# Optimization experiments

Measured on AMD Instinct MI355X. Metric: run time of the kernel, lower is better.

The kernel has to match this reference:

```python
import jax, jax.numpy as jnp
import numpy as np

B, N = 4096, 128
STATE_DIM, GOAL_DIM, OBSTACLE_DIM = 6, 6, 4
VEH = 2 * STATE_DIM + GOAL_DIM  # 18


def setup_inputs() -> dict:
    key = jax.random.key(0)
    ks = jax.random.split(key, 8)
    s = lambda k, shp, fan: jax.random.normal(k, shp, jnp.float32) / np.sqrt(fan)
    return {
        "obs": jax.random.normal(ks[0], (B, 138), jnp.float32),
        "obstacles": jax.random.uniform(ks[1], (B, 5, N), jnp.float32),
        "act": jax.random.normal(ks[2], (B, 2), jnp.float32),
        "ow1": s(ks[3], (22, 256), 22),
        "ob1": jnp.zeros((256,), jnp.float32),
        "ow2": s(ks[4], (256, 256), 256),
        "ob2": jnp.zeros((256,), jnp.float32),
        "qw1": s(ks[5], (396, 256), 396),
        "qb1": jnp.zeros((256,), jnp.float32),
        "qw2": s(ks[6], (256, 256), 256),
        "qb2": jnp.zeros((256,), jnp.float32),
        "qw3": s(ks[7], (256, 1), 256),
        "qb3": jnp.zeros((1,), jnp.float32),
    }


def reference(obs, obstacles, act, ow1, ob1, ow2, ob2, qw1, qb1, qw2, qb2, qw3, qb3):
    # obs: [B, 138]; obstacles: [B, obstacle_dim+1, N]; act: [B, 2]
    veh = obs[:, :VEH]                                 # [B, 18]
    obst_data = obstacles[:, :OBSTACLE_DIM, :]         # [B, 4, N]
    mask = obstacles[:, -1, :]                         # [B, N]
    # per-obstacle features: concat broadcast vehicle state with obstacle data -> [B, N, 22]
    x = jnp.concatenate(
        [jnp.broadcast_to(veh[:, None, :], (veh.shape[0], obst_data.shape[2], VEH)),
         obst_data.transpose(0, 2, 1)], axis=-1)
    # shared obstacle MLP (ReLU on both layers, incl. output_activation)
    h = jax.nn.relu(jnp.einsum("bnf,fh->bnh", x, ow1) + ob1)
    h = jax.nn.relu(jnp.einsum("bnh,hk->bnk", h, ow2) + ob2)  # [B, N, 256]
    # masked sum-pool over obstacle axis
    pooled = jnp.einsum("bnh,bn->bh", h, mask)         # [B, 256]
    comb = jnp.concatenate([obs, pooled, act], axis=-1)  # [B, 396]
    q = jax.nn.relu(comb @ qw1 + qb1)
    q = jax.nn.relu(q @ qw2 + qb2)
    q = q @ qw3 + qb3                                   # [B, 1]
    return jnp.squeeze(q, -1)
```

## Files before the change

kernel.cpp:

```cpp
#include <hip/hip_runtime.h>
#include <hip/hip_bf16.h>


typedef __attribute__((ext_vector_type(8))) short short8;
typedef __attribute__((ext_vector_type(4))) float f32x4;

#define MFMA16(A, B, C) __builtin_amdgcn_mfma_f32_16x16x32_bf16(A, B, C, 0, 0, 0)

__device__ __forceinline__ unsigned short f2b(float f) {
  __hip_bfloat16 h = __float2bfloat16(f);
  return __builtin_bit_cast(unsigned short, h);
}
__device__ __forceinline__ float b2f(unsigned short u) {
  unsigned v = ((unsigned)u) << 16;
  return __builtin_bit_cast(float, v);
}
__device__ __forceinline__ unsigned pk2f(float a, float b) {
  unsigned ua = __builtin_bit_cast(unsigned, a) + 0x8000u;
  unsigned ub = __builtin_bit_cast(unsigned, b) + 0x8000u;
  return __builtin_amdgcn_perm(ub, ua, 0x07060302u);
}

__global__ __launch_bounds__(256) void pack_weights(
    const float* __restrict__ ow1, const float* __restrict__ ow2,
    const float* __restrict__ qw1, const float* __restrict__ qw2,
    unsigned short* __restrict__ ow1q, unsigned short* __restrict__ ow2p,
    unsigned short* __restrict__ qw1h, unsigned short* __restrict__ qw1l,
    unsigned short* __restrict__ qw2h, unsigned short* __restrict__ qw2l) {
  int i = blockIdx.x * 256 + threadIdx.x;
  if (i < 8192) {
    int j = i & 7;
    int l15 = (i >> 3) & 15;
    int quad = (i >> 7) & 3;
    int mt = (i >> 9) & 15;
    int k = quad * 8 + j;
    float v = (k < 22) ? ow1[k * 256 + (mt * 16 + l15)] : 0.f;
    ow1q[i] = f2b(v);
  }
  if (i < 65536) {
    int j = i & 7;
    int n = (i >> 3) & 255;
    int qq = i >> 11;
    int k = (qq >> 2) * 32 + (qq & 3) * 8 + j;
    ow2p[i] = f2b(ow2[k * 256 + n]);
    float w = qw2[k * 256 + n];
    unsigned short h = f2b(w);
    qw2h[i] = h;
    qw2l[i] = f2b(w - b2f(h));
  }
  if (i < 106496) {
    int j = i & 7;
    int n = (i >> 3) & 255;
    int qq = i >> 11;
    int k = (qq >> 2) * 32 + (qq & 3) * 8 + j;
    float w = (k < 396) ? qw1[k * 256 + n] : 0.f;
    unsigned short h = f2b(w);
    qw1h[i] = h;
    qw1l[i] = f2b(w - b2f(h));
  }
}

#define XSTR 40
#define HSTR 272

__global__ __launch_bounds__(512, 4) void obstacle_kernel(
    const float* __restrict__ obs, const float* __restrict__ obstacles,
    const unsigned short* __restrict__ ow1q,
    const unsigned short* __restrict__ ow2p,
    const float* __restrict__ ob1, const float* __restrict__ ob2,
    unsigned short* __restrict__ poolH, unsigned short* __restrict__ poolL) {
  __shared__ __align__(16) unsigned short xs[128 * XSTR];
  __shared__ __align__(16) unsigned short h1[128 * HSTR];
  __shared__ float maskS[128];
  __shared__ unsigned short vehB[32];

  const int b = blockIdx.x;
  const int tid = threadIdx.x;

  if (tid < 18) vehB[tid] = f2b(obs[b * 138 + tid]);
  if (tid < 128) maskS[tid] = obstacles[b * 640 + 512 + tid];
  __syncthreads();

  if (tid < 256) {
    int n = tid >> 1;
    int half = tid & 1;
    unsigned short* wr = &xs[n * XSTR + half * 16];
    if (half == 0) {
      unsigned short r01[16];
#pragma unroll
      for (int k = 0; k < 16; k++) r01[k] = vehB[k];
      *(short8*)(wr + 0) = *(short8*)&r01[0];
      *(short8*)(wr + 8) = *(short8*)&r01[8];
    } else {
      unsigned short r2[8];
      r2[0] = vehB[16];
      r2[1] = vehB[17];
#pragma unroll
      for (int d = 0; d < 4; d++)
        r2[2 + d] = f2b(obstacles[b * 640 + d * 128 + n]);
      r2[6] = 0; r2[7] = 0;
      *(short8*)(wr + 0) = *(short8*)&r2[0];
      short8 z = {0, 0, 0, 0, 0, 0, 0, 0};
      *(short8*)(wr + 8) = z;
    }
  }
  __syncthreads();

  const int wave = tid >> 6;
  const int lane = tid & 63;
  const int quad = lane >> 4;
  const int l15 = lane & 15;

  {
    const unsigned short* wp = &ow1q[wave * 1024 + quad * 128 + l15 * 8];
    short8 wfr[2];
#pragma unroll
    for (int i = 0; i < 2; i++) wfr[i] = *(const short8*)(wp + i * 512);

    const unsigned short* bxp = &xs[l15 * XSTR + quad * 8];
    short8 bx[8];
#pragma unroll
    for (int nt = 0; nt < 8; nt++)
      bx[nt] = *(const short8*)(bxp + nt * 16 * XSTR);

    unsigned short* wrb = &h1[l15 * HSTR + wave * 32 + quad * 4];

#pragma unroll
    for (int i = 0; i < 2; i++) {
      f32x4 cinit = *(const f32x4*)&ob1[wave * 32 + i * 16 + quad * 4];
      f32x4 acc1[8];
#pragma unroll
      for (int nt = 0; nt < 8; nt++) acc1[nt] = MFMA16(wfr[i], bx[nt], cinit);
#pragma unroll
      for (int nt = 0; nt < 8; nt++) {
        float v0 = fmaxf(acc1[nt][0], 0.f);
        float v1 = fmaxf(acc1[nt][1], 0.f);
        float v2 = fmaxf(acc1[nt][2], 0.f);
        float v3 = fmaxf(acc1[nt][3], 0.f);
        uint2 pk;
        pk.x = pk2f(v0, v1);
        pk.y = pk2f(v2, v3);
        *(uint2*)(wrb + nt * 16 * HSTR + i * 16) = pk;
      }
    }
  }
  __syncthreads();

  f32x4 acc[8][2];
#pragma unroll
  for (int t = 0; t < 2; t++) {
    float bv = ob2[wave * 32 + t * 16 + l15];
    f32x4 bvec = {bv, bv, bv, bv};
#pragma unroll
    for (int mt = 0; mt < 8; mt++) acc[mt][t] = bvec;
  }

  const unsigned short* bp = &ow2p[(quad * 256 + wave * 32 + l15) * 8];
  const unsigned short* h1r = &h1[l15 * HSTR + quad * 8];
  short8 bcur[2], bnxt[2];
#pragma unroll
  for (int t = 0; t < 2; t++) bcur[t] = *(const short8*)(bp + t * 128);

#pragma unroll 1
  for (int kb = 0; kb < 8; kb++) {
    if (kb < 7) {
#pragma unroll
      for (int t = 0; t < 2; t++)
        bnxt[t] = *(const short8*)(bp + 8192 + t * 128);
    }
    short8 afr[8];
#pragma unroll
    for (int mt = 0; mt < 8; mt++)
      afr[mt] = *(const short8*)(h1r + mt * 16 * HSTR);
#pragma unroll
    for (int mt = 0; mt < 8; mt++)
#pragma unroll
      for (int t = 0; t < 2; t++) acc[mt][t] = MFMA16(afr[mt], bcur[t], acc[mt][t]);
    bp += 8192;
    h1r += 32;
    if (kb < 7) {
#pragma unroll
      for (int t = 0; t < 2; t++) bcur[t] = bnxt[t];
    }
  }

  f32x4 mk[8];
  const float* mkp = &maskS[quad * 4];
#pragma unroll
  for (int mt = 0; mt < 8; mt++) mk[mt] = *(const f32x4*)(mkp + mt * 16);

#pragma unroll
  for (int t = 0; t < 2; t++) {
    float s = 0.f;
#pragma unroll
    for (int mt = 0; mt < 8; mt++) {
#pragma unroll
      for (int r = 0; r < 4; r++) {
        float v = fmaxf(acc[mt][t][r], 0.f);
        s = fmaf(mk[mt][r], v, s);
      }
    }
    s += __shfl_xor(s, 16);
    s += __shfl_xor(s, 32);
    if (quad == 0) {
      int n = wave * 32 + t * 16 + l15;
      unsigned short sh = (unsigned short)(__builtin_bit_cast(unsigned, s) >> 16);
      poolH[b * 256 + n] = sh;
      poolL[b * 256 + n] = f2b(s - b2f(sh));
    }
  }
}

__global__ __launch_bounds__(1024) void head_mfma(
    const float* __restrict__ obs, const float* __restrict__ act,
    const unsigned short* __restrict__ poolH,
    const unsigned short* __restrict__ poolL,
    const unsigned short* __restrict__ qw1h,
    const unsigned short* __restrict__ qw1l,
    const unsigned short* __restrict__ qw2h,
    const unsigned short* __restrict__ qw2l,
    const float* __restrict__ qb1, const float* __restrict__ qb2,
    const float* __restrict__ qw3, const float* __restrict__ qb3,
    float* __restrict__ out) {
  const int CSTR = 424;
  const int HSTRQ = 264;
  __shared__ unsigned short combH[16 * 424], combL[16 * 424];
  __shared__ unsigned short h1H[16 * 264], h1L[16 * 264];
  __shared__ float wred[16][16];

  const int tid = threadIdx.x;
  const int r0 = blockIdx.x * 16;

  for (int idx = tid; idx < 16 * 416; idx += 1024) {
    int m = idx / 416;
    int k = idx - m * 416;
    unsigned short hi, lo;
    if (k < 138) {
      float v = obs[(r0 + m) * 138 + k];
      hi = f2b(v);
      lo = f2b(v - b2f(hi));
    } else if (k < 394) {
      hi = poolH[(r0 + m) * 256 + (k - 138)];
      lo = poolL[(r0 + m) * 256 + (k - 138)];
    } else if (k < 396) {
      float v = act[(r0 + m) * 2 + (k - 394)];
      hi = f2b(v);
      lo = f2b(v - b2f(hi));
    } else {
      hi = 0; lo = 0;
    }
    combH[m * CSTR + k] = hi;
    combL[m * CSTR + k] = lo;
  }
  __syncthreads();

  const int wave = tid >> 6;
  const int lane = tid & 63;
  const int quad = lane >> 4;
  const int l15 = lane & 15;
  const int n = wave * 16 + l15;

  f32x4 acc = {0.f, 0.f, 0.f, 0.f}, accm = {0.f, 0.f, 0.f, 0.f};
#pragma unroll 1
  for (int kb = 0; kb < 13; kb++) {
    int ao = l15 * CSTR + kb * 32 + quad * 8;
    short8 ah = *(const short8*)&combH[ao];
    short8 al = *(const short8*)&combL[ao];
    int off = ((kb * 4 + quad) * 256 + n) * 8;
    short8 bh = *(const short8*)&qw1h[off];
    short8 bl = *(const short8*)&qw1l[off];
    acc = MFMA16(ah, bh, acc);
    accm = MFMA16(ah, bl, accm);
    accm = MFMA16(al, bh, accm);
  }
  {
    float bias = qb1[n];
#pragma unroll
    for (int r = 0; r < 4; r++) {
      int m = quad * 4 + r;
      float v = fmaxf(acc[r] + accm[r] + bias, 0.f);
      unsigned short hi = f2b(v);
      h1H[m * HSTRQ + n] = hi;
      h1L[m * HSTRQ + n] = f2b(v - b2f(hi));
    }
  }
  __syncthreads();

  f32x4 a2 = {0.f, 0.f, 0.f, 0.f}, a2m = {0.f, 0.f, 0.f, 0.f};
#pragma unroll 1
  for (int kb = 0; kb < 8; kb++) {
    int ao = l15 * HSTRQ + kb * 32 + quad * 8;
    short8 ah = *(const short8*)&h1H[ao];
    short8 al = *(const short8*)&h1L[ao];
    int off = ((kb * 4 + quad) * 256 + n) * 8;
    short8 bh = *(const short8*)&qw2h[off];
    short8 bl = *(const short8*)&qw2l[off];
    a2 = MFMA16(ah, bh, a2);
    a2m = MFMA16(ah, bl, a2m);
    a2m = MFMA16(al, bh, a2m);
  }

  {
    float w3 = qw3[n];
    float qb2n = qb2[n];
#pragma unroll
    for (int r = 0; r < 4; r++) {
      float v = fmaxf(a2[r] + a2m[r] + qb2n, 0.f);
      float s = v * w3;
      s += __shfl_xor(s, 1);
      s += __shfl_xor(s, 2);
      s += __shfl_xor(s, 4);
      s += __shfl_xor(s, 8);
      if (l15 == 0) wred[wave][quad * 4 + r] = s;
    }
  }
  __syncthreads();
  if (tid < 16) {
    float s = qb3[0];
#pragma unroll
    for (int w = 0; w < 16; w++) s += wred[w][tid];
    out[r0 + tid] = s;
  }
}

extern "C" void kernel_launch(void* const* d_in, const int* in_sizes, int n_in,
                              void* d_out, int out_size, void* d_ws, size_t ws_size,
                              hipStream_t stream) {
  const float* obs       = (const float*)d_in[0];
  const float* obstacles = (const float*)d_in[1];
  const float* act       = (const float*)d_in[2];
  const float* ow1       = (const float*)d_in[3];
  const float* ob1       = (const float*)d_in[4];
  const float* ow2       = (const float*)d_in[5];
  const float* ob2       = (const float*)d_in[6];
  const float* qw1       = (const float*)d_in[7];
  const float* qb1       = (const float*)d_in[8];
  const float* qw2       = (const float*)d_in[9];
  const float* qb2       = (const float*)d_in[10];
  const float* qw3       = (const float*)d_in[11];
  const float* qb3       = (const float*)d_in[12];
  float* out = (float*)d_out;

  unsigned short* ow1q = (unsigned short*)d_ws;
  unsigned short* ow2p = ow1q + 8192;
  unsigned short* qw1h = ow2p + 65536;
  unsigned short* qw1l = qw1h + 106496;
  unsigned short* qw2h = qw1l + 106496;
  unsigned short* qw2l = qw2h + 65536;
  unsigned short* poolH = qw2l + 65536;
  unsigned short* poolL = poolH + 1048576;

  pack_weights<<<416, 256, 0, stream>>>(ow1, ow2, qw1, qw2, ow1q, ow2p, qw1h,
                                        qw1l, qw2h, qw2l);
  obstacle_kernel<<<4096, 512, 0, stream>>>(obs, obstacles, ow1q, ow2p, ob1,
                                            ob2, poolH, poolL);
  head_mfma<<<256, 1024, 0, stream>>>(obs, act, poolH, poolL, qw1h, qw1l,
                                      qw2h, qw2l, qb1, qb2, qw3, qb3, out);
}
```

Measured before the change: 167.5 us.

## Restructure head MLP kernel: 8 rows per block, two N-tiles per wave, prefetched weights

The head kernel now runs 512 blocks of 512 threads, each handling 8 batch rows padded into a 16-row MFMA tile. Each wave computes two 16-column output tiles, and weight fragments are double-buffered in registers so global loads for the next k-steps are issued ahead of the MFMAs. Layer-2 weight prefetch is also hoisted before the barrier, and the LDS stride for h1 changes. The aim is more blocks across the CUs and hidden weight-load latency, at the cost of wasting half of each MFMA tile on zero rows and extra register pressure.

Result: slower. 172.7 us (+3.1%).

```diff
diff --git a/kernel.cpp b/kernel.cpp
--- a/kernel.cpp
+++ b/kernel.cpp
@@ -211,7 +211,7 @@
   }
 }
 
-__global__ __launch_bounds__(1024) void head_mfma(
+__global__ __launch_bounds__(512) void head_mfma(
     const float* __restrict__ obs, const float* __restrict__ act,
     const unsigned short* __restrict__ poolH,
     const unsigned short* __restrict__ poolL,
@@ -223,99 +223,163 @@
     const float* __restrict__ qw3, const float* __restrict__ qb3,
     float* __restrict__ out) {
   const int CSTR = 424;
-  const int HSTRQ = 264;
+  const int HSTRQ = 272;
   __shared__ unsigned short combH[16 * 424], combL[16 * 424];
-  __shared__ unsigned short h1H[16 * 264], h1L[16 * 264];
+  __shared__ unsigned short h1H[16 * 272], h1L[16 * 272];
   __shared__ float wred[16][16];
 
   const int tid = threadIdx.x;
-  const int r0 = blockIdx.x * 16;
-
-  for (int idx = tid; idx < 16 * 416; idx += 1024) {
-    int m = idx / 416;
-    int k = idx - m * 416;
-    unsigned short hi, lo;
-    if (k < 138) {
-      float v = obs[(r0 + m) * 138 + k];
-      hi = f2b(v);
-      lo = f2b(v - b2f(hi));
-    } else if (k < 394) {
-      hi = poolH[(r0 + m) * 256 + (k - 138)];
-      lo = poolL[(r0 + m) * 256 + (k - 138)];
-    } else if (k < 396) {
-      float v = act[(r0 + m) * 2 + (k - 394)];
-      hi = f2b(v);
-      lo = f2b(v - b2f(hi));
-    } else {
-      hi = 0; lo = 0;
-    }
-    combH[m * CSTR + k] = hi;
-    combL[m * CSTR + k] = lo;
-  }
-  __syncthreads();
-
+  const int r0 = blockIdx.x * 8;
   const int wave = tid >> 6;
   const int lane = tid & 63;
   const int quad = lane >> 4;
   const int l15 = lane & 15;
-  const int n = wave * 16 + l15;
-
-  f32x4 acc = {0.f, 0.f, 0.f, 0.f}, accm = {0.f, 0.f, 0.f, 0.f};
-#pragma unroll 1
+  const int n0 = wave * 32 + l15;
+  const int n1 = wave * 32 + 16 + l15;
+
+  const unsigned short* w1h0 = &qw1h[(quad * 256 + n0) * 8];
+  const unsigned short* w1l0 = &qw1l[(quad * 256 + n0) * 8];
+  const unsigned short* w1h1 = &qw1h[(quad * 256 + n1) * 8];
+  const unsigned short* w1l1 = &qw1l[(quad * 256 + n1) * 8];
+
+  short8 bh0[2], bl0[2], bh1[2], bl1[2];
+  bh0[0] = *(const short8*)(w1h0);
+  bl0[0] = *(const short8*)(w1l0);
+  bh0[1] = *(const short8*)(w1h0 + 8192);
+  bl0[1] = *(const short8*)(w1l0 + 8192);
+  bh1[0] = *(const short8*)(w1h1);
+  bl1[0] = *(const short8*)(w1l1);
+  bh1[1] = *(const short8*)(w1h1 + 8192);
+  bl1[1] = *(const short8*)(w1l1 + 8192);
+
+  for (int idx = tid; idx < 16 * 416; idx += 512) {
+    int m = idx / 416;
+    int k = idx - m * 416;
+    unsigned short hi = 0, lo = 0;
+    if (m < 8) {
+      if (k < 138) {
+        float v = obs[(r0 + m) * 138 + k];
+        hi = f2b(v);
+        lo = f2b(v - b2f(hi));
+      } else if (k < 394) {
+        hi = poolH[(r0 + m) * 256 + (k - 138)];
+        lo = poolL[(r0 + m) * 256 + (k - 138)];
+      } else if (k < 396) {
+        float v = act[(r0 + m) * 2 + (k - 394)];
+        hi = f2b(v);
+        lo = f2b(v - b2f(hi));
+      }
+    }
+    combH[m * CSTR + k] = hi;
+    combL[m * CSTR + k] = lo;
+  }
+  __syncthreads();
+
+  f32x4 acc0 = {0.f, 0.f, 0.f, 0.f}, accm0 = {0.f, 0.f, 0.f, 0.f};
+  f32x4 acc1 = {0.f, 0.f, 0.f, 0.f}, accm1 = {0.f, 0.f, 0.f, 0.f};
+#pragma unroll
   for (int kb = 0; kb < 13; kb++) {
+    const int c = kb & 1;
+    short8 ch0 = bh0[c], cl0 = bl0[c];
+    short8 ch1 = bh1[c], cl1 = bl1[c];
+    if (kb + 2 < 13) {
+      bh0[c] = *(const short8*)(w1h0 + (kb + 2) * 8192);
+      bl0[c] = *(const short8*)(w1l0 + (kb + 2) * 8192);
+      bh1[c] = *(const short8*)(w1h1 + (kb + 2) * 8192);
+      bl1[c] = *(const short8*)(w1l1 + (kb + 2) * 8192);
+    }
     int ao = l15 * CSTR + kb * 32 + quad * 8;
     short8 ah = *(const short8*)&combH[ao];
     short8 al = *(const short8*)&combL[ao];
-    int off = ((kb * 4 + quad) * 256 + n) * 8;
-    short8 bh = *(const short8*)&qw1h[off];
-    short8 bl = *(const short8*)&qw1l[off];
-    acc = MFMA16(ah, bh, acc);
-    accm = MFMA16(ah, bl, accm);
-    accm = MFMA16(al, bh, accm);
+    acc0 = MFMA16(ah, ch0, acc0);
+    accm0 = MFMA16(ah, cl0, accm0);
+    accm0 = MFMA16(al, ch0, accm0);
+    acc1 = MFMA16(ah, ch1, acc1);
+    accm1 = MFMA16(ah, cl1, accm1);
+    accm1 = MFMA16(al, ch1, accm1);
   }
   {
-    float bias = qb1[n];
+    float bias0 = qb1[n0];
+    float bias1 = qb1[n1];
 #pragma unroll
     for (int r = 0; r < 4; r++) {
       int m = quad * 4 + r;
-      float v = fmaxf(acc[r] + accm[r] + bias, 0.f);
-      unsigned short hi = f2b(v);
-      h1H[m * HSTRQ + n] = hi;
-      h1L[m * HSTRQ + n] = f2b(v - b2f(hi));
-    }
-  }
-  __syncthreads();
-
-  f32x4 a2 = {0.f, 0.f, 0.f, 0.f}, a2m = {0.f, 0.f, 0.f, 0.f};
-#pragma unroll 1
+      float v0 = fmaxf(acc0[r] + accm0[r] + bias0, 0.f);
+      unsigned short hi0 = f2b(v0);
+      h1H[m * HSTRQ + n0] = hi0;
+      h1L[m * HSTRQ + n0] = f2b(v0 - b2f(hi0));
+      float v1 = fmaxf(acc1[r] + accm1[r] + bias1, 0.f);
+      unsigned short hi1 = f2b(v1);
+      h1H[m * HSTRQ + n1] = hi1;
+      h1L[m * HSTRQ + n1] = f2b(v1 - b2f(hi1));
+    }
+  }
+
+  const unsigned short* w2h0 = &qw2h[(quad * 256 + n0) * 8];
+  const unsigned short* w2l0 = &qw2l[(quad * 256 + n0) * 8];
+  const unsigned short* w2h1 = &qw2h[(quad * 256 + n1) * 8];
+  const unsigned short* w2l1 = &qw2l[(quad * 256 + n1) * 8];
+  short8 dh0[2], dl0[2], dh1[2], dl1[2];
+  dh0[0] = *(const short8*)(w2h0);
+  dl0[0] = *(const short8*)(w2l0);
+  dh0[1] = *(const short8*)(w2h0 + 8192);
+  dl0[1] = *(const short8*)(w2l0 + 8192);
+  dh1[0] = *(const short8*)(w2h1);
+  dl1[0] = *(const short8*)(w2l1);
+  dh1[1] = *(const short8*)(w2h1 + 8192);
+  dl1[1] = *(const short8*)(w2l1 + 8192);
+
+  __syncthreads();
+
+  f32x4 a20 = {0.f, 0.f, 0.f, 0.f}, a2m0 = {0.f, 0.f, 0.f, 0.f};
+  f32x4 a21 = {0.f, 0.f, 0.f, 0.f}, a2m1 = {0.f, 0.f, 0.f, 0.f};
+#pragma unroll
   for (int kb = 0; kb < 8; kb++) {
+    const int c = kb & 1;
+    short8 ch0 = dh0[c], cl0 = dl0[c];
+    short8 ch1 = dh1[c], cl1 = dl1[c];
+    if (kb + 2 < 8) {
+      dh0[c] = *(const short8*)(w2h0 + (kb + 2) * 8192);
+      dl0[c] = *(const short8*)(w2l0 + (kb + 2) * 8192);
+      dh1[c] = *(const short8*)(w2h1 + (kb + 2) * 8192);
+      dl1[c] = *(const short8*)(w2l1 + (kb + 2) * 8192);
+    }
     int ao = l15 * HSTRQ + kb * 32 + quad * 8;
     short8 ah = *(const short8*)&h1H[ao];
     short8 al = *(const short8*)&h1L[ao];
-    int off = ((kb * 4 + quad) * 256 + n) * 8;
-    short8 bh = *(const short8*)&qw2h[off];
-    short8 bl = *(const short8*)&qw2l[off];
-    a2 = MFMA16(ah, bh, a2);
-    a2m = MFMA16(ah, bl, a2m);
-    a2m = MFMA16(al, bh, a2m);
+    a20 = MFMA16(ah, ch0, a20);
+    a2m0 = MFMA16(ah, cl0, a2m0);
+    a2m0 = MFMA16(al, ch0, a2m0);
+    a21 = MFMA16(ah, ch1, a21);
+    a2m1 = MFMA16(ah, cl1, a2m1);
+    a2m1 = MFMA16(al, ch1, a2m1);
   }
 
   {
-    float w3 = qw3[n];
-    float qb2n = qb2[n];
+    float w30 = qw3[n0], w31 = qw3[n1];
+    float qb20 = qb2[n0], qb21 = qb2[n1];
 #pragma unroll
     for (int r = 0; r < 4; r++) {
-      float v = fmaxf(a2[r] + a2m[r] + qb2n, 0.f);
-      float s = v * w3;
-      s += __shfl_xor(s, 1);
-      s += __shfl_xor(s, 2);
-      s += __shfl_xor(s, 4);
-      s += __shfl_xor(s, 8);
-      if (l15 == 0) wred[wave][quad * 4 + r] = s;
-    }
-  }
-  __syncthreads();
-  if (tid < 16) {
+      float v0 = fmaxf(a20[r] + a2m0[r] + qb20, 0.f);
+      float s0 = v0 * w30;
+      s0 += __shfl_xor(s0, 1);
+      s0 += __shfl_xor(s0, 2);
+      s0 += __shfl_xor(s0, 4);
+      s0 += __shfl_xor(s0, 8);
+      float v1 = fmaxf(a21[r] + a2m1[r] + qb21, 0.f);
+      float s1 = v1 * w31;
+      s1 += __shfl_xor(s1, 1);
+      s1 += __shfl_xor(s1, 2);
+      s1 += __shfl_xor(s1, 4);
+      s1 += __shfl_xor(s1, 8);
+      if (l15 == 0) {
+        wred[wave * 2 + 0][quad * 4 + r] = s0;
+        wred[wave * 2 + 1][quad * 4 + r] = s1;
+      }
+    }
+  }
+  __syncthreads();
+  if (tid < 8) {
     float s = qb3[0];
 #pragma unroll
     for (int w = 0; w < 16; w++) s += wred[w][tid];
@@ -354,6 +418,6 @@
                                         qw1l, qw2h, qw2l);
   obstacle_kernel<<<4096, 512, 0, stream>>>(obs, obstacles, ow1q, ow2p, ob1,
                                             ob2, poolH, poolL);
-  head_mfma<<<256, 1024, 0, stream>>>(obs, act, poolH, poolL, qw1h, qw1l,
-                                      qw2h, qw2l, qb1, qb2, qw3, qb3, out);
-}
+  head_mfma<<<512, 512, 0, stream>>>(obs, act, poolH, poolL, qw1h, qw1l,
+                                     qw2h, qw2l, qb1, qb2, qw3, qb3, out);
+}
```

## Fuse obstacle and head kernels with per-group completion counters

Applied to the files above, without the earlier changes.

Merges the obstacle pooling kernel and the Q-head kernel into one launch. Head blocks are appended after the 4096 obstacle blocks and spin on an atomic counter until all 16 batch rows of their group are pooled, so head work can overlap the obstacle tail and one launch gap disappears. Pooled values are packed as hi/lo bf16 pairs in a single 32-bit store. The head now runs with 512 threads, each wave handling two 16-column tiles. It adds a memset, spin-wait overhead, and relies on dispatch order to avoid deadlock.

Result: slower. 202.6 us (+20.9%).

```diff
diff --git a/kernel.cpp b/kernel.cpp
--- a/kernel.cpp
+++ b/kernel.cpp
@@ -62,264 +62,301 @@
 
 #define XSTR 40
 #define HSTR 272
-
-__global__ __launch_bounds__(512, 4) void obstacle_kernel(
+#define CSTR 424
+#define HSTRQ 264
+
+__global__ __launch_bounds__(512, 4) void fused_kernel(
     const float* __restrict__ obs, const float* __restrict__ obstacles,
+    const float* __restrict__ act,
     const unsigned short* __restrict__ ow1q,
     const unsigned short* __restrict__ ow2p,
     const float* __restrict__ ob1, const float* __restrict__ ob2,
-    unsigned short* __restrict__ poolH, unsigned short* __restrict__ poolL) {
-  __shared__ __align__(16) unsigned short xs[128 * XSTR];
-  __shared__ __align__(16) unsigned short h1[128 * HSTR];
-  __shared__ float maskS[128];
-  __shared__ unsigned short vehB[32];
-
-  const int b = blockIdx.x;
-  const int tid = threadIdx.x;
-
-  if (tid < 18) vehB[tid] = f2b(obs[b * 138 + tid]);
-  if (tid < 128) maskS[tid] = obstacles[b * 640 + 512 + tid];
-  __syncthreads();
-
-  if (tid < 256) {
-    int n = tid >> 1;
-    int half = tid & 1;
-    unsigned short* wr = &xs[n * XSTR + half * 16];
-    if (half == 0) {
-      unsigned short r01[16];
-#pragma unroll
-      for (int k = 0; k < 16; k++) r01[k] = vehB[k];
-      *(short8*)(wr + 0) = *(short8*)&r01[0];
-      *(short8*)(wr + 8) = *(short8*)&r01[8];
-    } else {
-      unsigned short r2[8];
-      r2[0] = vehB[16];
-      r2[1] = vehB[17];
-#pragma unroll
-      for (int d = 0; d < 4; d++)
-        r2[2 + d] = f2b(obstacles[b * 640 + d * 128 + n]);
-      r2[6] = 0; r2[7] = 0;
-      *(short8*)(wr + 0) = *(short8*)&r2[0];
-      short8 z = {0, 0, 0, 0, 0, 0, 0, 0};
-      *(short8*)(wr + 8) = z;
-    }
-  }
-  __syncthreads();
-
-  const int wave = tid >> 6;
-  const int lane = tid & 63;
-  const int quad = lane >> 4;
-  const int l15 = lane & 15;
-
-  {
-    const unsigned short* wp = &ow1q[wave * 1024 + quad * 128 + l15 * 8];
-    short8 wfr[2];
-#pragma unroll
-    for (int i = 0; i < 2; i++) wfr[i] = *(const short8*)(wp + i * 512);
-
-    const unsigned short* bxp = &xs[l15 * XSTR + quad * 8];
-    short8 bx[8];
-#pragma unroll
-    for (int nt = 0; nt < 8; nt++)
-      bx[nt] = *(const short8*)(bxp + nt * 16 * XSTR);
-
-    unsigned short* wrb = &h1[l15 * HSTR + wave * 32 + quad * 4];
-
-#pragma unroll
-    for (int i = 0; i < 2; i++) {
-      f32x4 cinit = *(const f32x4*)&ob1[wave * 32 + i * 16 + quad * 4];
-      f32x4 acc1[8];
-#pragma unroll
-      for (int nt = 0; nt < 8; nt++) acc1[nt] = MFMA16(wfr[i], bx[nt], cinit);
-#pragma unroll
-      for (int nt = 0; nt < 8; nt++) {
-        float v0 = fmaxf(acc1[nt][0], 0.f);
-        float v1 = fmaxf(acc1[nt][1], 0.f);
-        float v2 = fmaxf(acc1[nt][2], 0.f);
-        float v3 = fmaxf(acc1[nt][3], 0.f);
-        uint2 pk;
-        pk.x = pk2f(v0, v1);
-        pk.y = pk2f(v2, v3);
-        *(uint2*)(wrb + nt * 16 * HSTR + i * 16) = pk;
-      }
-    }
-  }
-  __syncthreads();
-
-  f32x4 acc[8][2];
-#pragma unroll
-  for (int t = 0; t < 2; t++) {
-    float bv = ob2[wave * 32 + t * 16 + l15];
-    f32x4 bvec = {bv, bv, bv, bv};
-#pragma unroll
-    for (int mt = 0; mt < 8; mt++) acc[mt][t] = bvec;
-  }
-
-  const unsigned short* bp = &ow2p[(quad * 256 + wave * 32 + l15) * 8];
-  const unsigned short* h1r = &h1[l15 * HSTR + quad * 8];
-  short8 bcur[2], bnxt[2];
-#pragma unroll
-  for (int t = 0; t < 2; t++) bcur[t] = *(const short8*)(bp + t * 128);
-
-#pragma unroll 1
-  for (int kb = 0; kb < 8; kb++) {
-    if (kb < 7) {
-#pragma unroll
-      for (int t = 0; t < 2; t++)
-        bnxt[t] = *(const short8*)(bp + 8192 + t * 128);
-    }
-    short8 afr[8];
-#pragma unroll
-    for (int mt = 0; mt < 8; mt++)
-      afr[mt] = *(const short8*)(h1r + mt * 16 * HSTR);
-#pragma unroll
-    for (int mt = 0; mt < 8; mt++)
-#pragma unroll
-      for (int t = 0; t < 2; t++) acc[mt][t] = MFMA16(afr[mt], bcur[t], acc[mt][t]);
-    bp += 8192;
-    h1r += 32;
-    if (kb < 7) {
-#pragma unroll
-      for (int t = 0; t < 2; t++) bcur[t] = bnxt[t];
-    }
-  }
-
-  f32x4 mk[8];
-  const float* mkp = &maskS[quad * 4];
-#pragma unroll
-  for (int mt = 0; mt < 8; mt++) mk[mt] = *(const f32x4*)(mkp + mt * 16);
-
-#pragma unroll
-  for (int t = 0; t < 2; t++) {
-    float s = 0.f;
-#pragma unroll
-    for (int mt = 0; mt < 8; mt++) {
-#pragma unroll
-      for (int r = 0; r < 4; r++) {
-        float v = fmaxf(acc[mt][t][r], 0.f);
-        s = fmaf(mk[mt][r], v, s);
-      }
-    }
-    s += __shfl_xor(s, 16);
-    s += __shfl_xor(s, 32);
-    if (quad == 0) {
-      int n = wave * 32 + t * 16 + l15;
-      unsigned short sh = (unsigned short)(__builtin_bit_cast(unsigned, s) >> 16);
-      poolH[b * 256 + n] = sh;
-      poolL[b * 256 + n] = f2b(s - b2f(sh));
-    }
-  }
-}
-
-__global__ __launch_bounds__(1024) void head_mfma(
-    const float* __restrict__ obs, const float* __restrict__ act,
-    const unsigned short* __restrict__ poolH,
-    const unsigned short* __restrict__ poolL,
     const unsigned short* __restrict__ qw1h,
     const unsigned short* __restrict__ qw1l,
     const unsigned short* __restrict__ qw2h,
     const unsigned short* __restrict__ qw2l,
     const float* __restrict__ qb1, const float* __restrict__ qb2,
     const float* __restrict__ qw3, const float* __restrict__ qb3,
+    unsigned* __restrict__ pool32, unsigned* __restrict__ done,
     float* __restrict__ out) {
-  const int CSTR = 424;
-  const int HSTRQ = 264;
-  __shared__ unsigned short combH[16 * 424], combL[16 * 424];
-  __shared__ unsigned short h1H[16 * 264], h1L[16 * 264];
-  __shared__ float wred[16][16];
-
+  __shared__ __align__(16) char smem[80448];
   const int tid = threadIdx.x;
-  const int r0 = blockIdx.x * 16;
-
-  for (int idx = tid; idx < 16 * 416; idx += 1024) {
-    int m = idx / 416;
-    int k = idx - m * 416;
-    unsigned short hi, lo;
-    if (k < 138) {
-      float v = obs[(r0 + m) * 138 + k];
-      hi = f2b(v);
-      lo = f2b(v - b2f(hi));
-    } else if (k < 394) {
-      hi = poolH[(r0 + m) * 256 + (k - 138)];
-      lo = poolL[(r0 + m) * 256 + (k - 138)];
-    } else if (k < 396) {
-      float v = act[(r0 + m) * 2 + (k - 394)];
-      hi = f2b(v);
-      lo = f2b(v - b2f(hi));
-    } else {
-      hi = 0; lo = 0;
-    }
-    combH[m * CSTR + k] = hi;
-    combL[m * CSTR + k] = lo;
-  }
-  __syncthreads();
-
   const int wave = tid >> 6;
   const int lane = tid & 63;
   const int quad = lane >> 4;
   const int l15 = lane & 15;
-  const int n = wave * 16 + l15;
-
-  f32x4 acc = {0.f, 0.f, 0.f, 0.f}, accm = {0.f, 0.f, 0.f, 0.f};
+
+  if (blockIdx.x < 4096) {
+    unsigned short* xs = (unsigned short*)smem;
+    unsigned short* h1 = (unsigned short*)(smem + 10240);
+    float* maskS = (float*)(smem + 79872);
+    unsigned short* vehB = (unsigned short*)(smem + 80384);
+
+    const int b = blockIdx.x;
+
+    if (tid < 18) vehB[tid] = f2b(obs[b * 138 + tid]);
+    if (tid < 128) maskS[tid] = obstacles[b * 640 + 512 + tid];
+    __syncthreads();
+
+    if (tid < 256) {
+      int n = tid >> 1;
+      int half = tid & 1;
+      unsigned short* wr = &xs[n * XSTR + half * 16];
+      if (half == 0) {
+        unsigned short r01[16];
+#pragma unroll
+        for (int k = 0; k < 16; k++) r01[k] = vehB[k];
+        *(short8*)(wr + 0) = *(short8*)&r01[0];
+        *(short8*)(wr + 8) = *(short8*)&r01[8];
+      } else {
+        unsigned short r2[8];
+        r2[0] = vehB[16];
+        r2[1] = vehB[17];
+#pragma unroll
+        for (int d = 0; d < 4; d++)
+          r2[2 + d] = f2b(obstacles[b * 640 + d * 128 + n]);
+        r2[6] = 0; r2[7] = 0;
+        *(short8*)(wr + 0) = *(short8*)&r2[0];
+        short8 z = {0, 0, 0, 0, 0, 0, 0, 0};
+        *(short8*)(wr + 8) = z;
+      }
+    }
+    __syncthreads();
+
+    {
+      const unsigned short* wp = &ow1q[wave * 1024 + quad * 128 + l15 * 8];
+      short8 wfr[2];
+#pragma unroll
+      for (int i = 0; i < 2; i++) wfr[i] = *(const short8*)(wp + i * 512);
+
+      const unsigned short* bxp = &xs[l15 * XSTR + quad * 8];
+      short8 bx[8];
+#pragma unroll
+      for (int nt = 0; nt < 8; nt++)
+        bx[nt] = *(const short8*)(bxp + nt * 16 * XSTR);
+
+      unsigned short* wrb = &h1[l15 * HSTR + wave * 32 + quad * 4];
+
+#pragma unroll
+      for (int i = 0; i < 2; i++) {
+        f32x4 cinit = *(const f32x4*)&ob1[wave * 32 + i * 16 + quad * 4];
+        f32x4 acc1[8];
+#pragma unroll
+        for (int nt = 0; nt < 8; nt++) acc1[nt] = MFMA16(wfr[i], bx[nt], cinit);
+#pragma unroll
+        for (int nt = 0; nt < 8; nt++) {
+          float v0 = fmaxf(acc1[nt][0], 0.f);
+          float v1 = fmaxf(acc1[nt][1], 0.f);
+          float v2 = fmaxf(acc1[nt][2], 0.f);
+          float v3 = fmaxf(acc1[nt][3], 0.f);
+          uint2 pk;
+          pk.x = pk2f(v0, v1);
+          pk.y = pk2f(v2, v3);
+          *(uint2*)(wrb + nt * 16 * HSTR + i * 16) = pk;
+        }
+      }
+    }
+    __syncthreads();
+
+    f32x4 acc[8][2];
+#pragma unroll
+    for (int t = 0; t < 2; t++) {
+      float bv = ob2[wave * 32 + t * 16 + l15];
+      f32x4 bvec = {bv, bv, bv, bv};
+#pragma unroll
+      for (int mt = 0; mt < 8; mt++) acc[mt][t] = bvec;
+    }
+
+    const unsigned short* bp = &ow2p[(quad * 256 + wave * 32 + l15) * 8];
+    const unsigned short* h1r = &h1[l15 * HSTR + quad * 8];
+    short8 bcur[2], bnxt[2];
+#pragma unroll
+    for (int t = 0; t < 2; t++) bcur[t] = *(const short8*)(bp + t * 128);
+
 #pragma unroll 1
-  for (int kb = 0; kb < 13; kb++) {
-    int ao = l15 * CSTR + kb * 32 + quad * 8;
-    short8 ah = *(const short8*)&combH[ao];
-    short8 al = *(const short8*)&combL[ao];
-    int off = ((kb * 4 + quad) * 256 + n) * 8;
-    short8 bh = *(const short8*)&qw1h[off];
-    short8 bl = *(const short8*)&qw1l[off];
-    acc = MFMA16(ah, bh, acc);
-    accm = MFMA16(ah, bl, accm);
-    accm = MFMA16(al, bh, accm);
-  }
-  {
-    float bias = qb1[n];
-#pragma unroll
-    for (int r = 0; r < 4; r++) {
-      int m = quad * 4 + r;
-      float v = fmaxf(acc[r] + accm[r] + bias, 0.f);
-      unsigned short hi = f2b(v);
-      h1H[m * HSTRQ + n] = hi;
-      h1L[m * HSTRQ + n] = f2b(v - b2f(hi));
-    }
-  }
-  __syncthreads();
-
-  f32x4 a2 = {0.f, 0.f, 0.f, 0.f}, a2m = {0.f, 0.f, 0.f, 0.f};
+    for (int kb = 0; kb < 8; kb++) {
+      if (kb < 7) {
+#pragma unroll
+        for (int t = 0; t < 2; t++)
+          bnxt[t] = *(const short8*)(bp + 8192 + t * 128);
+      }
+      short8 afr[8];
+#pragma unroll
+      for (int mt = 0; mt < 8; mt++)
+        afr[mt] = *(const short8*)(h1r + mt * 16 * HSTR);
+#pragma unroll
+      for (int mt = 0; mt < 8; mt++)
+#pragma unroll
+        for (int t = 0; t < 2; t++) acc[mt][t] = MFMA16(afr[mt], bcur[t], acc[mt][t]);
+      bp += 8192;
+      h1r += 32;
+      if (kb < 7) {
+#pragma unroll
+        for (int t = 0; t < 2; t++) bcur[t] = bnxt[t];
+      }
+    }
+
+    f32x4 mk[8];
+    const float* mkp = &maskS[quad * 4];
+#pragma unroll
+    for (int mt = 0; mt < 8; mt++) mk[mt] = *(const f32x4*)(mkp + mt * 16);
+
+#pragma unroll
+    for (int t = 0; t < 2; t++) {
+      float s = 0.f;
+#pragma unroll
+      for (int mt = 0; mt < 8; mt++) {
+#pragma unroll
+        for (int r = 0; r < 4; r++) {
+          float v = fmaxf(acc[mt][t][r], 0.f);
+          s = fmaf(mk[mt][r], v, s);
+        }
+      }
+      s += __shfl_xor(s, 16);
+      s += __shfl_xor(s, 32);
+      if (quad == 0) {
+        int n = wave * 32 + t * 16 + l15;
+        unsigned short sh = (unsigned short)(__builtin_bit_cast(unsigned, s) >> 16);
+        unsigned short lo = f2b(s - b2f(sh));
+        unsigned pk = (unsigned)sh | ((unsigned)lo << 16);
+        __hip_atomic_store(&pool32[b * 256 + n], pk, __ATOMIC_RELAXED,
+                           __HIP_MEMORY_SCOPE_AGENT);
+      }
+    }
+    __syncthreads();
+    if (tid == 0)
+      __hip_atomic_fetch_add(&done[b >> 4], 1u, __ATOMIC_RELEASE,
+                             __HIP_MEMORY_SCOPE_AGENT);
+  } else {
+    unsigned short* combH = (unsigned short*)smem;
+    unsigned short* combL = (unsigned short*)(smem + 13568);
+    unsigned short* h1H = (unsigned short*)(smem + 27136);
+    unsigned short* h1L = (unsigned short*)(smem + 35584);
+    float(*wred)[16] = (float(*)[16])(smem + 44032);
+
+    const int g = blockIdx.x - 4096;
+    const int r0 = g * 16;
+    const int n0 = wave * 32 + l15;
+    const int n1 = n0 + 16;
+
+    if (tid == 0) {
+      while (__hip_atomic_load(&done[g], __ATOMIC_ACQUIRE,
+                               __HIP_MEMORY_SCOPE_AGENT) < 16u)
+        __builtin_amdgcn_s_sleep(2);
+    }
+    __syncthreads();
+
+    for (int idx = tid; idx < 16 * 416; idx += 512) {
+      int m = idx / 416;
+      int k = idx - m * 416;
+      unsigned short hi = 0, lo = 0;
+      if (k < 138) {
+        float v = obs[(r0 + m) * 138 + k];
+        hi = f2b(v);
+        lo = f2b(v - b2f(hi));
+      } else if (k < 394) {
+        unsigned u = __hip_atomic_load(&pool32[(r0 + m) * 256 + (k - 138)],
+                                       __ATOMIC_RELAXED,
+                                       __HIP_MEMORY_SCOPE_AGENT);
+        hi = (unsigned short)u;
+        lo = (unsigned short)(u >> 16);
+      } else if (k < 396) {
+        float v = act[(r0 + m) * 2 + (k - 394)];
+        hi = f2b(v);
+        lo = f2b(v - b2f(hi));
+      }
+      combH[m * CSTR + k] = hi;
+      combL[m * CSTR + k] = lo;
+    }
+    __syncthreads();
+
+    f32x4 ac0 = {0.f, 0.f, 0.f, 0.f}, am0 = {0.f, 0.f, 0.f, 0.f};
+    f32x4 ac1 = {0.f, 0.f, 0.f, 0.f}, am1 = {0.f, 0.f, 0.f, 0.f};
 #pragma unroll 1
-  for (int kb = 0; kb < 8; kb++) {
-    int ao = l15 * HSTRQ + kb * 32 + quad * 8;
-    short8 ah = *(const short8*)&h1H[ao];
-    short8 al = *(const short8*)&h1L[ao];
-    int off = ((kb * 4 + quad) * 256 + n) * 8;
-    short8 bh = *(const short8*)&qw2h[off];
-    short8 bl = *(const short8*)&qw2l[off];
-    a2 = MFMA16(ah, bh, a2);
-    a2m = MFMA16(ah, bl, a2m);
-    a2m = MFMA16(al, bh, a2m);
-  }
-
-  {
-    float w3 = qw3[n];
-    float qb2n = qb2[n];
-#pragma unroll
-    for (int r = 0; r < 4; r++) {
-      float v = fmaxf(a2[r] + a2m[r] + qb2n, 0.f);
-      float s = v * w3;
-      s += __shfl_xor(s, 1);
-      s += __shfl_xor(s, 2);
-      s += __shfl_xor(s, 4);
-      s += __shfl_xor(s, 8);
-      if (l15 == 0) wred[wave][quad * 4 + r] = s;
-    }
-  }
-  __syncthreads();
-  if (tid < 16) {
-    float s = qb3[0];
-#pragma unroll
-    for (int w = 0; w < 16; w++) s += wred[w][tid];
-    out[r0 + tid] = s;
+    for (int kb = 0; kb < 13; kb++) {
+      int ao = l15 * CSTR + kb * 32 + quad * 8;
+      short8 ah = *(const short8*)&combH[ao];
+      short8 al = *(const short8*)&combL[ao];
+      int off = ((kb * 4 + quad) * 256 + n0) * 8;
+      short8 bh0 = *(const short8*)&qw1h[off];
+      short8 bl0 = *(const short8*)&qw1l[off];
+      short8 bh1 = *(const short8*)&qw1h[off + 128];
+      short8 bl1 = *(const short8*)&qw1l[off + 128];
+      ac0 = MFMA16(ah, bh0, ac0);
+      am0 = MFMA16(ah, bl0, am0);
+      am0 = MFMA16(al, bh0, am0);
+      ac1 = MFMA16(ah, bh1, ac1);
+      am1 = MFMA16(ah, bl1, am1);
+      am1 = MFMA16(al, bh1, am1);
+    }
+    {
+      float bias0 = qb1[n0];
+      float bias1 = qb1[n1];
+#pragma unroll
+      for (int r = 0; r < 4; r++) {
+        int m = quad * 4 + r;
+        float v0 = fmaxf(ac0[r] + am0[r] + bias0, 0.f);
+        unsigned short hi0 = f2b(v0);
+        h1H[m * HSTRQ + n0] = hi0;
+        h1L[m * HSTRQ + n0] = f2b(v0 - b2f(hi0));
+        float v1 = fmaxf(ac1[r] + am1[r] + bias1, 0.f);
+        unsigned short hi1 = f2b(v1);
+        h1H[m * HSTRQ + n1] = hi1;
+        h1L[m * HSTRQ + n1] = f2b(v1 - b2f(hi1));
+      }
+    }
+    __syncthreads();
+
+    f32x4 b20 = {0.f, 0.f, 0.f, 0.f}, bm0 = {0.f, 0.f, 0.f, 0.f};
+    f32x4 b21 = {0.f, 0.f, 0.f, 0.f}, bm1 = {0.f, 0.f, 0.f, 0.f};
+#pragma unroll 1
+    for (int kb = 0; kb < 8; kb++) {
+      int ao = l15 * HSTRQ + kb * 32 + quad * 8;
+      short8 ah = *(const short8*)&h1H[ao];
+      short8 al = *(const short8*)&h1L[ao];
+      int off = ((kb * 4 + quad) * 256 + n0) * 8;
+      short8 bh0 = *(const short8*)&qw2h[off];
+      short8 bl0 = *(const short8*)&qw2l[off];
+      short8 bh1 = *(const short8*)&qw2h[off + 128];
+      short8 bl1 = *(const short8*)&qw2l[off + 128];
+      b20 = MFMA16(ah, bh0, b20);
+      bm0 = MFMA16(ah, bl0, bm0);
+      bm0 = MFMA16(al, bh0, bm0);
+      b21 = MFMA16(ah, bh1, b21);
+      bm1 = MFMA16(ah, bl1, bm1);
+      bm1 = MFMA16(al, bh1, bm1);
+    }
+
+    {
+      float w30 = qw3[n0], w31 = qw3[n1];
+      float qb20 = qb2[n0], qb21 = qb2[n1];
+#pragma unroll
+      for (int r = 0; r < 4; r++) {
+        float v0 = fmaxf(b20[r] + bm0[r] + qb20, 0.f);
+        float s0 = v0 * w30;
+        s0 += __shfl_xor(s0, 1);
+        s0 += __shfl_xor(s0, 2);
+        s0 += __shfl_xor(s0, 4);
+        s0 += __shfl_xor(s0, 8);
+        float v1 = fmaxf(b21[r] + bm1[r] + qb21, 0.f);
+        float s1 = v1 * w31;
+        s1 += __shfl_xor(s1, 1);
+        s1 += __shfl_xor(s1, 2);
+        s1 += __shfl_xor(s1, 4);
+        s1 += __shfl_xor(s1, 8);
+        if (l15 == 0) {
+          wred[wave * 2 + 0][quad * 4 + r] = s0;
+          wred[wave * 2 + 1][quad * 4 + r] = s1;
+        }
+      }
+    }
+    __syncthreads();
+    if (tid < 16) {
+      float s = qb3[0];
+#pragma unroll
+      for (int w = 0; w < 16; w++) s += wred[w][tid];
+      out[r0 + tid] = s;
+    }
   }
 }
 
@@ -347,13 +384,13 @@
   unsigned short* qw1l = qw1h + 106496;
   unsigned short* qw2h = qw1l + 106496;
   unsigned short* qw2l = qw2h + 65536;
-  unsigned short* poolH = qw2l + 65536;
-  unsigned short* poolL = poolH + 1048576;
-
+  unsigned* pool32 = (unsigned*)(qw2l + 65536);
+  unsigned* done = pool32 + 4096 * 256;
+
+  hipMemsetAsync(done, 0, 256 * sizeof(unsigned), stream);
   pack_weights<<<416, 256, 0, stream>>>(ow1, ow2, qw1, qw2, ow1q, ow2p, qw1h,
                                         qw1l, qw2h, qw2l);
-  obstacle_kernel<<<4096, 512, 0, stream>>>(obs, obstacles, ow1q, ow2p, ob1,
-                                            ob2, poolH, poolL);
-  head_mfma<<<256, 1024, 0, stream>>>(obs, act, poolH, poolL, qw1h, qw1l,
-                                      qw2h, qw2l, qb1, qb2, qw3, qb3, out);
-}
+  fused_kernel<<<4352, 512, 0, stream>>>(obs, obstacles, act, ow1q, ow2p, ob1,
+                                         ob2, qw1h, qw1l, qw2h, qw2l, qb1, qb2,
+                                         qw3, qb3, pool32, done, out);
+}
```

## Start layer-2 K loop on wave-owned h1 slice before barrier

Applied to the files above, without the earlier changes.

Each wave writes its own 32-column slice of h1 in layer 1, so the layer-2 K loop is rotated to start at the block the wave itself produced. That first K-block is consumed before the __syncthreads, and the remaining seven blocks follow the barrier in rotated order. The ow2 prefetch is also issued before layer 1 to hide global latency. This is meant to overlap barrier wait with MFMA work, at the cost of a staggered access order across waves and more register pressure from the early prefetch.

Measured after the change: 166.9 us, median of 2. About the same (-0.3%).

```diff
diff --git a/kernel.cpp b/kernel.cpp
--- a/kernel.cpp
+++ b/kernel.cpp
@@ -111,6 +111,12 @@
   const int quad = lane >> 4;
   const int l15 = lane & 15;
 
+  const unsigned short* bbase = &ow2p[(quad * 256 + wave * 32 + l15) * 8];
+  short8 bcur[2], bnxt[2];
+#pragma unroll
+  for (int t = 0; t < 2; t++)
+    bcur[t] = *(const short8*)(bbase + wave * 8192 + t * 128);
+
   {
     const unsigned short* wp = &ow1q[wave * 1024 + quad * 128 + l15 * 8];
     short8 wfr[2];
@@ -144,7 +150,6 @@
       }
     }
   }
-  __syncthreads();
 
   f32x4 acc[8][2];
 #pragma unroll
@@ -155,30 +160,43 @@
     for (int mt = 0; mt < 8; mt++) acc[mt][t] = bvec;
   }
 
-  const unsigned short* bp = &ow2p[(quad * 256 + wave * 32 + l15) * 8];
-  const unsigned short* h1r = &h1[l15 * HSTR + quad * 8];
-  short8 bcur[2], bnxt[2];
-#pragma unroll
-  for (int t = 0; t < 2; t++) bcur[t] = *(const short8*)(bp + t * 128);
+  const unsigned short* h1base = &h1[l15 * HSTR + quad * 8];
+
+  {
+    const int kb = wave;
+#pragma unroll
+    for (int t = 0; t < 2; t++)
+      bnxt[t] = *(const short8*)(bbase + (((kb + 1) & 7) * 8192) + t * 128);
+    short8 afr[8];
+#pragma unroll
+    for (int mt = 0; mt < 8; mt++)
+      afr[mt] = *(const short8*)(h1base + kb * 32 + mt * 16 * HSTR);
+#pragma unroll
+    for (int mt = 0; mt < 8; mt++)
+#pragma unroll
+      for (int t = 0; t < 2; t++) acc[mt][t] = MFMA16(afr[mt], bcur[t], acc[mt][t]);
+#pragma unroll
+    for (int t = 0; t < 2; t++) bcur[t] = bnxt[t];
+  }
+  __syncthreads();
 
 #pragma unroll 1
-  for (int kb = 0; kb < 8; kb++) {
-    if (kb < 7) {
+  for (int j = 1; j < 8; j++) {
+    const int kb = (wave + j) & 7;
+    if (j < 7) {
 #pragma unroll
       for (int t = 0; t < 2; t++)
-        bnxt[t] = *(const short8*)(bp + 8192 + t * 128);
+        bnxt[t] = *(const short8*)(bbase + (((kb + 1) & 7) * 8192) + t * 128);
     }
     short8 afr[8];
 #pragma unroll
     for (int mt = 0; mt < 8; mt++)
-      afr[mt] = *(const short8*)(h1r + mt * 16 * HSTR);
+      afr[mt] = *(const short8*)(h1base + kb * 32 + mt * 16 * HSTR);
 #pragma unroll
     for (int mt = 0; mt < 8; mt++)
 #pragma unroll
       for (int t = 0; t < 2; t++) acc[mt][t] = MFMA16(afr[mt], bcur[t], acc[mt][t]);
-    bp += 8192;
-    h1r += 32;
-    if (kb < 7) {
+    if (j < 7) {
 #pragma unroll
       for (int t = 0; t < 2; t++) bcur[t] = bnxt[t];
     }
```
